# Performance work log

Hardware: AMD Instinct MI355X
Metric: run time of the kernel (lower is better)

## Reference

```python
import jax, jax.numpy as jnp
import numpy as np


def setup_inputs() -> dict:
    key = jax.random.key(0)
    ks = jax.random.split(key, 11)
    C = 256
    s = 1.0 / np.sqrt(C)
    x = jax.random.normal(ks[0], (8, C, 128, 128), jnp.float32)
    v_w = jax.random.normal(ks[1], (C, C), jnp.float32) * s      # v_conv 1x1: C->C
    v_b = jax.random.normal(ks[2], (C,), jnp.float32) * 0.01
    k_w = jax.random.normal(ks[3], (C,), jnp.float32) * s        # k_conv 1x1: C->1
    k_b = jax.random.normal(ks[4], (), jnp.float32) * 0.01
    w1 = jax.random.normal(ks[5], (2,), jnp.float32) * 0.7       # conv1 1x1: 2->1 (h branch)
    b1 = jax.random.normal(ks[6], (), jnp.float32) * 0.01
    w2 = jax.random.normal(ks[7], (2,), jnp.float32) * 0.7       # conv2 1x1: 2->1 (w branch)
    b2 = jax.random.normal(ks[8], (), jnp.float32) * 0.01
    w3 = jax.random.normal(ks[9], (C,), jnp.float32) * s         # conv3 1x1: C->1
    b3 = jax.random.normal(ks[10], (), jnp.float32) * 0.01
    return dict(x=x, v_w=v_w, v_b=v_b, k_w=k_w, k_b=k_b,
                w1=w1, b1=b1, w2=w2, b2=b2, w3=w3, b3=b3)


def reference(x, v_w, v_b, k_w, k_b, w1, b1, w2, b2, w3, b3):
    b, c, h, w = x.shape
    # v_conv (1x1) and k_conv (1x1 -> single channel)
    tmp = jnp.einsum('oc,bchw->bohw', v_w, x) + v_b[None, :, None, None]
    k = (jnp.einsum('c,bchw->bhw', k_w, x) + k_b).reshape(b, h * w)
    k = jax.nn.softmax(k, axis=1)                                # softmax over spatial
    channel_fea = jnp.einsum('bcn,bn->bc', tmp.reshape(b, c, h * w), k)  # [b,c]
    # h branch: adaptive max/avg pool over (c, w) per height row
    h_max = jnp.max(x, axis=(1, 3))                              # [b,h]
    h_avg = jnp.mean(x, axis=(1, 3))                             # [b,h]
    h_att = jax.nn.sigmoid(w1[0] * h_max + w1[1] * h_avg + b1)   # [b,h]
    # w branch: adaptive max/avg pool over (c, h) per width column
    w_max = jnp.max(x, axis=(1, 2))                              # [b,w]
    w_avg = jnp.mean(x, axis=(1, 2))                             # [b,w]
    w_att = jax.nn.sigmoid(w2[0] * w_max + w2[1] * w_avg + b2)   # [b,w]
    # spatial_fea = h_att*tmp + w_att*tmp, fused as tmp*(h_att+w_att)
    spatial = tmp * (h_att[:, None, :, None] + w_att[:, None, None, :])
    s = jax.nn.sigmoid(jnp.einsum('c,bchw->bhw', w3, spatial) + b3)  # [b,h,w]
    return s[:, None, :, :] * channel_fea[:, :, None, None] + x
```

## Files before the change

kernel.cpp:

```cpp
#include <hip/hip_runtime.h>
#include <math.h>

#define CC   256
#define NN   16384
#define NB   8
#define TILE 512
#define NT   32

#define WV3_OFF   0
#define WB3_OFF   256
#define S_OFF     264
#define HSUM_OFF  272
#define HMAX_OFF  1296
#define WSUM_OFF  2320
#define WMK_OFF   3344
#define XK_OFF    4368
#define CF_OFF    6416
#define HA_OFF    8464
#define WA_OFF    9488
#define T3_OFF    10512
#define ZERO_BYTES (6416*4)

__device__ __forceinline__ unsigned fkey(float f){
  unsigned b = __float_as_uint(f);
  return (b & 0x80000000u) ? ~b : (b ^ 0x80000000u);
}
__device__ __forceinline__ float fdekey(unsigned k){
  unsigned b = (k & 0x80000000u) ? (k ^ 0x80000000u) : ~k;
  return __uint_as_float(b);
}
__device__ __forceinline__ float sigmoidf_(float z){ return 1.0f/(1.0f+expf(-z)); }

__global__ __launch_bounds__(256) void k0(const float* __restrict__ v_w,
                                          const float* __restrict__ v_b,
                                          const float* __restrict__ w3,
                                          float* __restrict__ ws){
  const int t = threadIdx.x, g = blockIdx.x;
  float acc = 0.f;
  #pragma unroll
  for (int i=0;i<16;++i){
    int o = g*16 + i;
    acc += w3[o]*v_w[o*CC + t];
  }
  atomicAdd(ws + WV3_OFF + t, acc);
  if (g == 0){
    float v = w3[t]*v_b[t];
    #pragma unroll
    for (int m=1;m<=32;m<<=1) v += __shfl_xor(v, m, 64);
    __shared__ float l[4];
    if ((t&63)==0) l[t>>6] = v;
    __syncthreads();
    if (t==0) ws[WB3_OFF] = l[0]+l[1]+l[2]+l[3];
  }
}

__global__ __launch_bounds__(256) void k1(const float* __restrict__ x,
                                          const float* __restrict__ k_w,
                                          float* __restrict__ ws)
{
  const int t = threadIdx.x, lane = t&63, wv = t>>6;
  const int tile = blockIdx.x, b = blockIdx.y;
  const int n0 = tile*TILE;

  __shared__ float skw[CC], swv[CC];
  __shared__ float lred[4][128];
  __shared__ float sS[4];
  skw[t] = k_w[t];
  swv[t] = ws[WV3_OFF + t];
  __syncthreads();

  const float* xb = x + (size_t)b*CC*NN + n0 + 2*t;

  float kl0=0.f,kl1=0.f,t30=0.f,t31=0.f,cs0=0.f,cs1=0.f;
  float cm0=-INFINITY, cm1=-INFINITY;
  #pragma unroll 8
  for (int c=0;c<CC;++c){
    const float2 v = *(const float2*)(xb + (size_t)c*NN);
    const float kw = skw[c], wvv = swv[c];
    kl0 += kw*v.x;  kl1 += kw*v.y;
    t30 += wvv*v.x; t31 += wvv*v.y;
    cs0 += v.x;     cs1 += v.y;
    cm0 = fmaxf(cm0, v.x); cm1 = fmaxf(cm1, v.y);
  }

  *(float2*)(ws + T3_OFF + (size_t)b*NN + n0 + 2*t) = make_float2(t30, t31);

  float hs = cs0+cs1, hm = fmaxf(cm0, cm1);
  #pragma unroll
  for (int m=1;m<=32;m<<=1){
    hs += __shfl_xor(hs, m, 64);
    hm  = fmaxf(hm, __shfl_xor(hm, m, 64));
  }
  if (lane == 0){
    ws[HSUM_OFF + b*128 + tile*4 + wv] = hs;
    ws[HMAX_OFF + b*128 + tile*4 + wv] = hm;
  }

  lred[wv][2*lane] = cs0; lred[wv][2*lane+1] = cs1;
  __syncthreads();
  if (t < 128)
    atomicAdd(ws + WSUM_OFF + b*128 + t, lred[0][t]+lred[1][t]+lred[2][t]+lred[3][t]);
  __syncthreads();
  lred[wv][2*lane] = cm0; lred[wv][2*lane+1] = cm1;
  __syncthreads();
  if (t < 128){
    float m_ = fmaxf(fmaxf(lred[0][t],lred[1][t]), fmaxf(lred[2][t],lred[3][t]));
    atomicMax((unsigned*)ws + WMK_OFF + b*128 + t, fkey(m_));
  }

  const float e0 = expf(kl0), e1 = expf(kl1);
  float es = e0 + e1;
  #pragma unroll
  for (int m=1;m<=32;m<<=1) es += __shfl_xor(es, m, 64);
  if (lane == 0) sS[wv] = es;
  __syncthreads();
  if (t == 0) atomicAdd(ws + S_OFF + b, sS[0]+sS[1]+sS[2]+sS[3]);

  float xkacc0=0.f, xkacc1=0.f, xkacc2=0.f, xkacc3=0.f;
  #pragma unroll
  for (int cg=0; cg<4; ++cg){
    #pragma unroll 8
    for (int cl=0; cl<64; ++cl){
      const int c = cg*64 + cl;
      const float2 v = *(const float2*)(xb + (size_t)c*NN);
      float p = v.x*e0 + v.y*e1;
      #pragma unroll
      for (int m=1;m<=32;m<<=1) p += __shfl_xor(p, m, 64);
      if (lane == cl){
        if      (cg==0) xkacc0 = p;
        else if (cg==1) xkacc1 = p;
        else if (cg==2) xkacc2 = p;
        else            xkacc3 = p;
      }
    }
  }
  atomicAdd(ws + XK_OFF + b*CC +   0 + lane, xkacc0);
  atomicAdd(ws + XK_OFF + b*CC +  64 + lane, xkacc1);
  atomicAdd(ws + XK_OFF + b*CC + 128 + lane, xkacc2);
  atomicAdd(ws + XK_OFF + b*CC + 192 + lane, xkacc3);
}

__global__ __launch_bounds__(256) void k4(const float* __restrict__ v_w,
                                          const float* __restrict__ v_b,
                                          const float* __restrict__ w1, const float* __restrict__ b1,
                                          const float* __restrict__ w2, const float* __restrict__ b2,
                                          float* __restrict__ ws){
  const int b = blockIdx.x, t = threadIdx.x;
  const float inv = 1.0f/(256.0f*128.0f);
  if (t < 128){
    float hsum = ws[HSUM_OFF + b*128 + t] * inv;
    float hmax = ws[HMAX_OFF + b*128 + t];
    ws[HA_OFF + b*128 + t] = sigmoidf_(w1[0]*hmax + w1[1]*hsum + b1[0]);
  } else {
    int w = t - 128;
    float wsum = ws[WSUM_OFF + b*128 + w] * inv;
    float wmax = fdekey(((unsigned*)ws)[WMK_OFF + b*128 + w]);
    ws[WA_OFF + b*128 + w] = sigmoidf_(w2[0]*wmax + w2[1]*wsum + b2[0]);
  }
  __shared__ float xks[CC];
  const float Sinv = 1.0f / ws[S_OFF + b];
  xks[t] = ws[XK_OFF + b*CC + t] * Sinv;
  __syncthreads();
  float acc = v_b[t];
  #pragma unroll 8
  for (int c=0;c<CC;++c) acc += v_w[t*CC + c]*xks[c];
  ws[CF_OFF + b*CC + t] = acc;
}

__global__ __launch_bounds__(256) void k5(const float* __restrict__ x,
                                          const float* __restrict__ ws,
                                          const float* __restrict__ b3,
                                          float* __restrict__ out){
  const float4* x4 = (const float4*)x;
  float4* o4 = (float4*)out;
  const float4* t34 = (const float4*)(ws + T3_OFF);
  const float4* wa4 = (const float4*)(ws + WA_OFF);
  const float* ha = ws + HA_OFF;
  const float* cf = ws + CF_OFF;
  const float wb3 = ws[WB3_OFF];
  const float bb3 = b3[0];
  const int nq = NB*CC*NN/4;
  for (int q = blockIdx.x*256 + threadIdx.x; q < nq; q += gridDim.x*256){
    const int bc = q >> 12;
    const int b  = bc >> 8;
    const int n4 = q & 4095;
    const float f = cf[bc];
    const float hav = ha[b*128 + (n4>>5)];
    const float4 wav = wa4[b*32 + (n4&31)];
    const float4 tv = t34[(size_t)b*4096 + n4];
    const float4 xv = x4[q];
    float4 r;
    r.x = sigmoidf_((hav+wav.x)*(tv.x+wb3)+bb3)*f + xv.x;
    r.y = sigmoidf_((hav+wav.y)*(tv.y+wb3)+bb3)*f + xv.y;
    r.z = sigmoidf_((hav+wav.z)*(tv.z+wb3)+bb3)*f + xv.z;
    r.w = sigmoidf_((hav+wav.w)*(tv.w+wb3)+bb3)*f + xv.w;
    o4[q] = r;
  }
}

extern "C" void kernel_launch(void* const* d_in, const int* in_sizes, int n_in,
                              void* d_out, int out_size, void* d_ws, size_t ws_size,
                              hipStream_t stream) {
  const float* x   = (const float*)d_in[0];
  const float* v_w = (const float*)d_in[1];
  const float* v_b = (const float*)d_in[2];
  const float* k_w = (const float*)d_in[3];
  const float* w1  = (const float*)d_in[5];
  const float* b1  = (const float*)d_in[6];
  const float* w2  = (const float*)d_in[7];
  const float* b2  = (const float*)d_in[8];
  const float* w3  = (const float*)d_in[9];
  const float* b3  = (const float*)d_in[10];
  float* ws  = (float*)d_ws;
  float* out = (float*)d_out;

  hipMemsetAsync(d_ws, 0, ZERO_BYTES, stream);
  k0<<<16, 256, 0, stream>>>(v_w, v_b, w3, ws);
  k1<<<dim3(NT, NB), 256, 0, stream>>>(x, k_w, ws);
  k4<<<NB, 256, 0, stream>>>(v_w, v_b, w1, b1, w2, b2, ws);
  k5<<<2048, 256, 0, stream>>>(x, ws, b3, out);
}
```

Before: 325.2 us.

## Split channel reduction across more blocks and compute softmax-weighted sums separately

The stats kernel is split over four channel chunks, so 1024 blocks run instead of 256. Per-chunk partial logits and t3 go to the output buffer as scratch, and a combine kernel then produces exp weights and the folded t3. The shuffle-heavy x·softmax pass becomes its own per-(b,c) float4 dot-product kernel, and the channel-feature matvec is spread over 32 blocks with coalesced float4 reads. This fixes the low occupancy of the old 256-block kernel and its serial shuffle reductions. In exchange it adds a second full read of x, extra launches, and more atomics.

Result: faster. 307.4 us (-5.5%).

```diff
diff --git a/kernel.cpp b/kernel.cpp
--- a/kernel.cpp
+++ b/kernel.cpp
@@ -6,20 +6,25 @@
 #define NB   8
 #define TILE 512
 #define NT   32
+#define NCH  4
+#define CHC  64
 
 #define WV3_OFF   0
 #define WB3_OFF   256
 #define S_OFF     264
 #define HSUM_OFF  272
-#define HMAX_OFF  1296
+#define HMK_OFF   1296
 #define WSUM_OFF  2320
 #define WMK_OFF   3344
-#define XK_OFF    4368
+#define ZERO_END  4368
+#define HA_OFF    4368
+#define WA_OFF    5392
 #define CF_OFF    6416
-#define HA_OFF    8464
-#define WA_OFF    9488
-#define T3_OFF    10512
-#define ZERO_BYTES (6416*4)
+#define XK_OFF    8464
+#define EK_OFF    16384
+#define T3C_OFF   (EK_OFF + NB*NN)
+#define OKLP_OFF  0
+#define OT3P_OFF  (NCH*NB*NN)
 
 __device__ __forceinline__ unsigned fkey(float f){
   unsigned b = __float_as_uint(f);
@@ -38,8 +43,8 @@
   const int t = threadIdx.x, g = blockIdx.x;
   float acc = 0.f;
   #pragma unroll
-  for (int i=0;i<16;++i){
-    int o = g*16 + i;
+  for (int i=0;i<4;++i){
+    int o = g*4 + i;
     acc += w3[o]*v_w[o*CC + t];
   }
   atomicAdd(ws + WV3_OFF + t, acc);
@@ -54,27 +59,29 @@
   }
 }
 
-__global__ __launch_bounds__(256) void k1(const float* __restrict__ x,
-                                          const float* __restrict__ k_w,
-                                          float* __restrict__ ws)
+__global__ __launch_bounds__(256) void k1a(const float* __restrict__ x,
+                                           const float* __restrict__ k_w,
+                                           float* __restrict__ ws,
+                                           float* __restrict__ oscratch)
 {
   const int t = threadIdx.x, lane = t&63, wv = t>>6;
-  const int tile = blockIdx.x, b = blockIdx.y;
-  const int n0 = tile*TILE;
-
-  __shared__ float skw[CC], swv[CC];
+  const int tile = blockIdx.x;
+  const int q    = blockIdx.y;
+  const int b    = blockIdx.z;
+  const int n0   = tile*TILE;
+  const int c0   = q*CHC;
+
+  __shared__ float skw[CHC], swv[CHC];
   __shared__ float lred[4][128];
-  __shared__ float sS[4];
-  skw[t] = k_w[t];
-  swv[t] = ws[WV3_OFF + t];
-  __syncthreads();
-
-  const float* xb = x + (size_t)b*CC*NN + n0 + 2*t;
+  if (t < CHC){ skw[t] = k_w[c0+t]; swv[t] = ws[WV3_OFF + c0 + t]; }
+  __syncthreads();
+
+  const float* xb = x + ((size_t)(b*CC + c0))*NN + n0 + 2*t;
 
   float kl0=0.f,kl1=0.f,t30=0.f,t31=0.f,cs0=0.f,cs1=0.f;
   float cm0=-INFINITY, cm1=-INFINITY;
   #pragma unroll 8
-  for (int c=0;c<CC;++c){
+  for (int c=0;c<CHC;++c){
     const float2 v = *(const float2*)(xb + (size_t)c*NN);
     const float kw = skw[c], wvv = swv[c];
     kl0 += kw*v.x;  kl1 += kw*v.y;
@@ -83,7 +90,9 @@
     cm0 = fmaxf(cm0, v.x); cm1 = fmaxf(cm1, v.y);
   }
 
-  *(float2*)(ws + T3_OFF + (size_t)b*NN + n0 + 2*t) = make_float2(t30, t31);
+  const size_t pidx = ((size_t)(q*NB + b))*NN + n0 + 2*t;
+  *(float2*)(oscratch + OKLP_OFF + pidx) = make_float2(kl0, kl1);
+  *(float2*)(oscratch + OT3P_OFF + pidx) = make_float2(t30, t31);
 
   float hs = cs0+cs1, hm = fmaxf(cm0, cm1);
   #pragma unroll
@@ -92,8 +101,8 @@
     hm  = fmaxf(hm, __shfl_xor(hm, m, 64));
   }
   if (lane == 0){
-    ws[HSUM_OFF + b*128 + tile*4 + wv] = hs;
-    ws[HMAX_OFF + b*128 + tile*4 + wv] = hm;
+    atomicAdd(ws + HSUM_OFF + b*128 + tile*4 + wv, hs);
+    atomicMax((unsigned*)ws + HMK_OFF + b*128 + tile*4 + wv, fkey(hm));
   }
 
   lred[wv][2*lane] = cs0; lred[wv][2*lane+1] = cs1;
@@ -107,37 +116,54 @@
     float m_ = fmaxf(fmaxf(lred[0][t],lred[1][t]), fmaxf(lred[2][t],lred[3][t]));
     atomicMax((unsigned*)ws + WMK_OFF + b*128 + t, fkey(m_));
   }
-
+}
+
+__global__ __launch_bounds__(256) void k1b(float* __restrict__ ws,
+                                           const float* __restrict__ oscratch){
+  const int chunk = blockIdx.x;
+  const int b = blockIdx.y;
+  const int t = threadIdx.x, lane = t&63, wv = t>>6;
+  const int n = chunk*512 + 2*t;
+  const float wb3 = ws[WB3_OFF];
+
+  float kl0=0.f,kl1=0.f,t30=0.f,t31=0.f;
+  #pragma unroll
+  for (int qq=0; qq<NCH; ++qq){
+    const size_t pidx = ((size_t)(qq*NB + b))*NN + n;
+    const float2 kv = *(const float2*)(oscratch + OKLP_OFF + pidx);
+    const float2 tv = *(const float2*)(oscratch + OT3P_OFF + pidx);
+    kl0 += kv.x; kl1 += kv.y; t30 += tv.x; t31 += tv.y;
+  }
   const float e0 = expf(kl0), e1 = expf(kl1);
+  *(float2*)(ws + EK_OFF  + (size_t)b*NN + n) = make_float2(e0, e1);
+  *(float2*)(ws + T3C_OFF + (size_t)b*NN + n) = make_float2(t30+wb3, t31+wb3);
+
   float es = e0 + e1;
   #pragma unroll
   for (int m=1;m<=32;m<<=1) es += __shfl_xor(es, m, 64);
+  __shared__ float sS[4];
   if (lane == 0) sS[wv] = es;
   __syncthreads();
   if (t == 0) atomicAdd(ws + S_OFF + b, sS[0]+sS[1]+sS[2]+sS[3]);
-
-  float xkacc0=0.f, xkacc1=0.f, xkacc2=0.f, xkacc3=0.f;
-  #pragma unroll
-  for (int cg=0; cg<4; ++cg){
-    #pragma unroll 8
-    for (int cl=0; cl<64; ++cl){
-      const int c = cg*64 + cl;
-      const float2 v = *(const float2*)(xb + (size_t)c*NN);
-      float p = v.x*e0 + v.y*e1;
-      #pragma unroll
-      for (int m=1;m<=32;m<<=1) p += __shfl_xor(p, m, 64);
-      if (lane == cl){
-        if      (cg==0) xkacc0 = p;
-        else if (cg==1) xkacc1 = p;
-        else if (cg==2) xkacc2 = p;
-        else            xkacc3 = p;
-      }
-    }
-  }
-  atomicAdd(ws + XK_OFF + b*CC +   0 + lane, xkacc0);
-  atomicAdd(ws + XK_OFF + b*CC +  64 + lane, xkacc1);
-  atomicAdd(ws + XK_OFF + b*CC + 128 + lane, xkacc2);
-  atomicAdd(ws + XK_OFF + b*CC + 192 + lane, xkacc3);
+}
+
+__global__ __launch_bounds__(256) void k3(const float* __restrict__ x,
+                                          float* __restrict__ ws){
+  const int c = blockIdx.x, b = blockIdx.y, t = threadIdx.x;
+  const float4* x4 = (const float4*)(x + ((size_t)(b*CC + c))*NN);
+  const float4* e4 = (const float4*)(ws + EK_OFF + (size_t)b*NN);
+  float acc = 0.f;
+  #pragma unroll 4
+  for (int j=t; j<NN/4; j+=256){
+    const float4 xv = x4[j], ev = e4[j];
+    acc += xv.x*ev.x + xv.y*ev.y + xv.z*ev.z + xv.w*ev.w;
+  }
+  #pragma unroll
+  for (int m=1;m<=32;m<<=1) acc += __shfl_xor(acc, m, 64);
+  __shared__ float l[4];
+  if ((t&63)==0) l[t>>6] = acc;
+  __syncthreads();
+  if (t==0) ws[XK_OFF + b*CC + c] = l[0]+l[1]+l[2]+l[3];
 }
 
 __global__ __launch_bounds__(256) void k4(const float* __restrict__ v_w,
@@ -145,26 +171,40 @@
                                           const float* __restrict__ w1, const float* __restrict__ b1,
                                           const float* __restrict__ w2, const float* __restrict__ b2,
                                           float* __restrict__ ws){
-  const int b = blockIdx.x, t = threadIdx.x;
-  const float inv = 1.0f/(256.0f*128.0f);
-  if (t < 128){
-    float hsum = ws[HSUM_OFF + b*128 + t] * inv;
-    float hmax = ws[HMAX_OFF + b*128 + t];
-    ws[HA_OFF + b*128 + t] = sigmoidf_(w1[0]*hmax + w1[1]*hsum + b1[0]);
-  } else {
-    int w = t - 128;
-    float wsum = ws[WSUM_OFF + b*128 + w] * inv;
-    float wmax = fdekey(((unsigned*)ws)[WMK_OFF + b*128 + w]);
-    ws[WA_OFF + b*128 + w] = sigmoidf_(w2[0]*wmax + w2[1]*wsum + b2[0]);
+  const int oc = blockIdx.x, b = blockIdx.y, t = threadIdx.x;
+  if (oc == 0){
+    const float inv = 1.0f/(256.0f*128.0f);
+    if (t < 128){
+      float hsum = ws[HSUM_OFF + b*128 + t] * inv;
+      float hmax = fdekey(((unsigned*)ws)[HMK_OFF + b*128 + t]);
+      ws[HA_OFF + b*128 + t] = sigmoidf_(w1[0]*hmax + w1[1]*hsum + b1[0]);
+    } else {
+      int w = t - 128;
+      float wsum = ws[WSUM_OFF + b*128 + w] * inv;
+      float wmax = fdekey(((unsigned*)ws)[WMK_OFF + b*128 + w]);
+      ws[WA_OFF + b*128 + w] = sigmoidf_(w2[0]*wmax + w2[1]*wsum + b2[0]);
+    }
   }
   __shared__ float xks[CC];
   const float Sinv = 1.0f / ws[S_OFF + b];
   xks[t] = ws[XK_OFF + b*CC + t] * Sinv;
   __syncthreads();
-  float acc = v_b[t];
-  #pragma unroll 8
-  for (int c=0;c<CC;++c) acc += v_w[t*CC + c]*xks[c];
-  ws[CF_OFF + b*CC + t] = acc;
+  const float4* xk4 = (const float4*)xks;
+
+  const int o  = oc*64 + (t>>2);
+  const int qq = t & 3;
+  const float4* vw4 = (const float4*)(v_w + (size_t)o*CC);
+  float acc = 0.f;
+  #pragma unroll
+  for (int i=0;i<16;++i){
+    const int c4 = qq + 4*i;
+    const float4 wv = vw4[c4];
+    const float4 xv = xk4[c4];
+    acc += wv.x*xv.x + wv.y*xv.y + wv.z*xv.z + wv.w*xv.w;
+  }
+  acc += __shfl_xor(acc, 1, 64);
+  acc += __shfl_xor(acc, 2, 64);
+  if (qq == 0) ws[CF_OFF + b*CC + o] = acc + v_b[o];
 }
 
 __global__ __launch_bounds__(256) void k5(const float* __restrict__ x,
@@ -173,11 +213,10 @@
                                           float* __restrict__ out){
   const float4* x4 = (const float4*)x;
   float4* o4 = (float4*)out;
-  const float4* t34 = (const float4*)(ws + T3_OFF);
+  const float4* t34 = (const float4*)(ws + T3C_OFF);
   const float4* wa4 = (const float4*)(ws + WA_OFF);
   const float* ha = ws + HA_OFF;
   const float* cf = ws + CF_OFF;
-  const float wb3 = ws[WB3_OFF];
   const float bb3 = b3[0];
   const int nq = NB*CC*NN/4;
   for (int q = blockIdx.x*256 + threadIdx.x; q < nq; q += gridDim.x*256){
@@ -190,10 +229,10 @@
     const float4 tv = t34[(size_t)b*4096 + n4];
     const float4 xv = x4[q];
     float4 r;
-    r.x = sigmoidf_((hav+wav.x)*(tv.x+wb3)+bb3)*f + xv.x;
-    r.y = sigmoidf_((hav+wav.y)*(tv.y+wb3)+bb3)*f + xv.y;
-    r.z = sigmoidf_((hav+wav.z)*(tv.z+wb3)+bb3)*f + xv.z;
-    r.w = sigmoidf_((hav+wav.w)*(tv.w+wb3)+bb3)*f + xv.w;
+    r.x = sigmoidf_((hav+wav.x)*tv.x + bb3)*f + xv.x;
+    r.y = sigmoidf_((hav+wav.y)*tv.y + bb3)*f + xv.y;
+    r.z = sigmoidf_((hav+wav.z)*tv.z + bb3)*f + xv.z;
+    r.w = sigmoidf_((hav+wav.w)*tv.w + bb3)*f + xv.w;
     o4[q] = r;
   }
 }
@@ -214,9 +253,11 @@
   float* ws  = (float*)d_ws;
   float* out = (float*)d_out;
 
-  hipMemsetAsync(d_ws, 0, ZERO_BYTES, stream);
-  k0<<<16, 256, 0, stream>>>(v_w, v_b, w3, ws);
-  k1<<<dim3(NT, NB), 256, 0, stream>>>(x, k_w, ws);
-  k4<<<NB, 256, 0, stream>>>(v_w, v_b, w1, b1, w2, b2, ws);
-  k5<<<2048, 256, 0, stream>>>(x, ws, b3, out);
-}
+  hipMemsetAsync(d_ws, 0, (size_t)ZERO_END*sizeof(float), stream);
+  k0 <<<64, 256, 0, stream>>>(v_w, v_b, w3, ws);
+  k1a<<<dim3(NT, NCH, NB), 256, 0, stream>>>(x, k_w, ws, out);
+  k1b<<<dim3(32, NB), 256, 0, stream>>>(ws, out);
+  k3 <<<dim3(CC, NB), 256, 0, stream>>>(x, ws);
+  k4 <<<dim3(4, NB), 256, 0, stream>>>(v_w, v_b, w1, b1, w2, b2, ws);
+  k5 <<<2048, 256, 0, stream>>>(x, ws, b3, out);
+}
```
